# Kernel tuning notes

Measured on AMD Instinct MI355X. Metric: run time of the kernel, lower is better.

## Reference

```python
import jax, jax.numpy as jnp
import numpy as np

B, D, H, O = 8192, 1024, 2048, 1024   # batch, input_dim, hidden_dim, output_dim
T, NOPS = 4, 3                        # num_tempers, operators per bank (fixed at init)


def setup_inputs() -> dict:
    key = jax.random.key(0)
    ks = jax.random.split(key, 6)
    sc = 0.02
    return {
        "x": jax.random.normal(ks[0], (B, D), jnp.float32),
        # per-temper input_proj: Linear(D -> H)
        "Wp": jax.random.normal(ks[1], (T, H, D), jnp.float32) * sc,
        "bp": jnp.zeros((T, H), jnp.float32),
        "Wop": jax.random.normal(ks[2], (T, NOPS, H, H), jnp.float32) * sc,
        "bop": jnp.zeros((T, NOPS, H), jnp.float32),
        # routing_logits ~ randn per Temper.__init__
        "logits": jax.random.normal(ks[3], (T, NOPS), jnp.float32),
        # readout: Linear(T*H -> O)
        "Wr": jax.random.normal(ks[4], (O, T * H), jnp.float32) * sc,
        "br": jnp.zeros((O,), jnp.float32),
    }


def reference(x, Wp, bp, Wop, bop, logits, Wr, br):
    def temper(Wp_i, bp_i, Wop_i, bop_i, lg):
        # input projection: [B, H]
        xp = x @ Wp_i.T + bp_i
        # top-2 routing over operator bank (output is unweighted dispatch)
        w = jax.nn.softmax(lg)
        _, idx = jax.lax.top_k(w, 2)
        Wa, ba = Wop_i[idx[0]], bop_i[idx[0]]
        Wb, bb = Wop_i[idx[1]], bop_i[idx[1]]
        # each operator = Sequential(ReLU, Linear, ReLU)
        h = jax.nn.relu(jax.nn.relu(xp) @ Wa.T + ba)
        return jax.nn.relu(jax.nn.relu(h) @ Wb.T + bb)

    outs = jax.vmap(temper)(Wp, bp, Wop, bop, logits)          # [T, B, H]
    cat = jnp.transpose(outs, (1, 0, 2)).reshape(x.shape[0], -1)  # [B, T*H]
    return cat @ Wr.T + br                                      # [B, O]
```

## Files before the change

kernel.cpp:

```cpp
#include <hip/hip_runtime.h>

static constexpr int Bn = 8192;
static constexpr int Dd = 1024;
static constexpr int Hh = 2048;
static constexpr int Oo = 1024;
static constexpr int Tt = 4;
static constexpr int NO = 3;
#define TB 256

typedef __attribute__((ext_vector_type(8))) short bf16x8;
typedef __attribute__((ext_vector_type(4))) float f32x4;

__device__ __forceinline__ ushort f2bf(float f) {
  union { float f; unsigned u; } v; v.f = f;
  return (ushort)((v.u + 0x7FFFu + ((v.u >> 16) & 1u)) >> 16);
}

__global__ void top2_kernel(const float* __restrict__ logits, int* __restrict__ idx) {
  if (threadIdx.x == 0 && blockIdx.x == 0) {
    for (int t = 0; t < Tt; ++t) {
      const float* lg = logits + t * NO;
      int i0 = 0;
      for (int k = 1; k < NO; ++k) if (lg[k] > lg[i0]) i0 = k;
      int i1 = -1;
      for (int k = 0; k < NO; ++k) {
        if (k == i0) continue;
        if (i1 < 0 || lg[k] > lg[i1]) i1 = k;
      }
      idx[2 * t] = i0;
      idx[2 * t + 1] = i1;
    }
  }
}

__global__ void cvt_bf16(const float* __restrict__ src, ushort* __restrict__ dst, int n4) {
  int i = blockIdx.x * blockDim.x + threadIdx.x;
  if (i >= n4) return;
  float4 v = ((const float4*)src)[i];
  ((ushort4*)dst)[i] = make_ushort4(f2bf(v.x), f2bf(v.y), f2bf(v.z), f2bf(v.w));
}

__global__ void cvt_sel(const float* __restrict__ WopT, const int* __restrict__ idx2,
                        ushort* __restrict__ Wa, ushort* __restrict__ Wb, int n4) {
  int i = blockIdx.x * blockDim.x + threadIdx.x;
  if (i >= n4) return;
  size_t n = (size_t)n4 * 4;
  float4 va = ((const float4*)(WopT + (size_t)idx2[0] * n))[i];
  float4 vb = ((const float4*)(WopT + (size_t)idx2[1] * n))[i];
  ((ushort4*)Wa)[i] = make_ushort4(f2bf(va.x), f2bf(va.y), f2bf(va.z), f2bf(va.w));
  ((ushort4*)Wb)[i] = make_ushort4(f2bf(vb.x), f2bf(vb.y), f2bf(vb.z), f2bf(vb.w));
}

#define ISSUE_TILE(kk, p)                                                                   \
  do {                                                                                      \
    __builtin_amdgcn_global_load_lds(                                                       \
        (const __attribute__((address_space(1))) void*)(a0 + (kk)),                         \
        (__attribute__((address_space(3))) void*)(&As[p][w * 512]), 16, 0, 0);              \
    __builtin_amdgcn_global_load_lds(                                                       \
        (const __attribute__((address_space(1))) void*)(a1 + (kk)),                         \
        (__attribute__((address_space(3))) void*)(&As[p][2048 + w * 512]), 16, 0, 0);       \
    __builtin_amdgcn_global_load_lds(                                                       \
        (const __attribute__((address_space(1))) void*)(b0 + (kk)),                         \
        (__attribute__((address_space(3))) void*)(&Bs[p][w * 512]), 16, 0, 0);              \
    __builtin_amdgcn_global_load_lds(                                                       \
        (const __attribute__((address_space(1))) void*)(b1 + (kk)),                         \
        (__attribute__((address_space(3))) void*)(&Bs[p][2048 + w * 512]), 16, 0, 0);       \
  } while (0)

template <int EP>
__global__ __launch_bounds__(TB) void gemm_bt(
    const ushort* __restrict__ A, int lda,
    const ushort* __restrict__ B, int ldb,
    const float* __restrict__ bias, const int* __restrict__ idxp, int sel, int bstride,
    void* __restrict__ Cv, int ldc, int K) {
  __shared__ __align__(16) ushort As[2][128 * 32];
  __shared__ __align__(16) ushort Bs[2][128 * 32];
  const int tid = threadIdx.x;
  const int w = tid >> 6;
  const int lane = tid & 63;
  const int quad = lane >> 4;
  const int l16 = lane & 15;

  const int GX = gridDim.x, GY = gridDim.y;
  const int f = blockIdx.y * GX + blockIdx.x;
  const int xcd = f & 7;
  const int s = f >> 3;
  const int pxc = (GX >= 16) ? 2 : 1;
  const int pw = GX / pxc;
  const int ph = (GY * pxc) >> 3;
  const int bx = (xcd % pxc) * pw + (s % pw);
  const int by = (xcd / pxc) * ph + (s / pw);
  const int m0 = by * 128;
  const int n0 = bx * 128;
  const int wm = (w >> 1) * 64;
  const int wn = (w & 1) * 64;

  f32x4 acc[4][4];
#pragma unroll
  for (int i = 0; i < 4; ++i)
#pragma unroll
    for (int j = 0; j < 4; ++j)
#pragma unroll
      for (int r = 0; r < 4; ++r) acc[i][j][r] = 0.f;

  const int srow = tid >> 2;
  const int skc = ((tid & 3) ^ ((tid >> 3) & 3)) * 8;
  const ushort* a0 = A + (size_t)(m0 + srow) * lda + skc;
  const ushort* a1 = A + (size_t)(m0 + 64 + srow) * lda + skc;
  const ushort* b0 = B + (size_t)(n0 + srow) * ldb + skc;
  const ushort* b1 = B + (size_t)(n0 + 64 + srow) * ldb + skc;

  const int fq = (quad ^ ((l16 >> 1) & 3)) * 8;

  const int niter = K >> 5;
  ISSUE_TILE(0, 0);
  for (int it = 0; it < niter; ++it) {
    const int p = it & 1;
    __syncthreads();
    if (it + 1 < niter) ISSUE_TILE((it + 1) << 5, p ^ 1);

    bf16x8 af[4], bfr[4];
#pragma unroll
    for (int i = 0; i < 4; ++i)
      af[i] = *(const bf16x8*)&As[p][((wm >> 4) + i) * 512 + l16 * 32 + fq];
#pragma unroll
    for (int j = 0; j < 4; ++j)
      bfr[j] = *(const bf16x8*)&Bs[p][((wn >> 4) + j) * 512 + l16 * 32 + fq];
#pragma unroll
    for (int i = 0; i < 4; ++i)
#pragma unroll
      for (int j = 0; j < 4; ++j)
        acc[i][j] = __builtin_amdgcn_mfma_f32_16x16x32_bf16(af[i], bfr[j], acc[i][j], 0, 0, 0);
  }

  const float* bb = bias;
  if (EP == 0 && idxp) bb += (size_t)idxp[sel] * bstride;

#pragma unroll
  for (int i = 0; i < 4; ++i) {
#pragma unroll
    for (int j = 0; j < 4; ++j) {
      const int col = n0 + wn + j * 16 + l16;
      const float bv = (EP == 2) ? 0.f : bb[col];
#pragma unroll
      for (int r = 0; r < 4; ++r) {
        const int row = m0 + wm + i * 16 + quad * 4 + r;
        float v = acc[i][j][r] + bv;
        if (EP == 0) {
          v = v > 0.f ? v : 0.f;
          ((ushort*)Cv)[(size_t)row * ldc + col] = f2bf(v);
        } else if (EP == 1) {
          ((float*)Cv)[(size_t)row * ldc + col] = v;
        } else {
          ((float*)Cv)[(size_t)row * ldc + col] += v;
        }
      }
    }
  }
}

extern "C" void kernel_launch(void* const* d_in, const int* in_sizes, int n_in,
                              void* d_out, int out_size, void* d_ws, size_t ws_size,
                              hipStream_t stream) {
  const float* x      = (const float*)d_in[0];
  const float* Wp     = (const float*)d_in[1];
  const float* bp     = (const float*)d_in[2];
  const float* Wop    = (const float*)d_in[3];
  const float* bop    = (const float*)d_in[4];
  const float* logits = (const float*)d_in[5];
  const float* Wr     = (const float*)d_in[6];
  const float* br     = (const float*)d_in[7];
  float* out = (float*)d_out;

  char* ws = (char*)d_ws;
  size_t off = 0;
  int* idx = (int*)ws;                          off += 256;
  ushort* xb   = (ushort*)(ws + off);           off += (size_t)Bn * Dd * 2;
  ushort* WpB  = (ushort*)(ws + off);           off += (size_t)Tt * Hh * Dd * 2;
  ushort* WrB  = (ushort*)(ws + off);           off += (size_t)Oo * Tt * Hh * 2;
  ushort* WaB  = (ushort*)(ws + off);           off += (size_t)Hh * Hh * 2;
  ushort* WbB  = (ushort*)(ws + off);           off += (size_t)Hh * Hh * 2;
  ushort* bufA = (ushort*)(ws + off);           off += (size_t)Bn * Hh * 2;
  ushort* bufB = (ushort*)(ws + off);           off += (size_t)Bn * Hh * 2;

  top2_kernel<<<1, 64, 0, stream>>>(logits, idx);
  {
    int n4 = Bn * Dd / 4;
    cvt_bf16<<<(n4 + TB - 1) / TB, TB, 0, stream>>>(x, xb, n4);
  }
  {
    int n4 = Tt * Hh * Dd / 4;
    cvt_bf16<<<(n4 + TB - 1) / TB, TB, 0, stream>>>(Wp, WpB, n4);
  }
  {
    int n4 = Oo * Tt * Hh / 4;
    cvt_bf16<<<(n4 + TB - 1) / TB, TB, 0, stream>>>(Wr, WrB, n4);
  }

  dim3 gHB(Hh / 128, Bn / 128);
  dim3 gOB(Oo / 128, Bn / 128);

  for (int t = 0; t < Tt; ++t) {
    int n4 = Hh * Hh / 4;
    cvt_sel<<<(n4 + TB - 1) / TB, TB, 0, stream>>>(Wop + (size_t)t * NO * Hh * Hh, idx + 2 * t,
                                                   WaB, WbB, n4);
    gemm_bt<0><<<gHB, TB, 0, stream>>>(xb, Dd, WpB + (size_t)t * Hh * Dd, Dd,
                                       bp + (size_t)t * Hh, nullptr, 0, 0, bufA, Hh, Dd);
    gemm_bt<0><<<gHB, TB, 0, stream>>>(bufA, Hh, WaB, Hh,
                                       bop + (size_t)t * NO * Hh, idx + 2 * t, 0, Hh,
                                       bufB, Hh, Hh);
    gemm_bt<0><<<gHB, TB, 0, stream>>>(bufB, Hh, WbB, Hh,
                                       bop + (size_t)t * NO * Hh, idx + 2 * t, 1, Hh,
                                       bufA, Hh, Hh);
    if (t == 0)
      gemm_bt<1><<<gOB, TB, 0, stream>>>(bufA, Hh, WrB + (size_t)t * Hh, Tt * Hh,
                                         br, nullptr, 0, 0, out, Oo, Hh);
    else
      gemm_bt<2><<<gOB, TB, 0, stream>>>(bufA, Hh, WrB + (size_t)t * Hh, Tt * Hh,
                                         nullptr, nullptr, 0, 0, out, Oo, Hh);
  }
}
```

Baseline: 1.464 ms.

## Add 256x256 8-wave GEMM with ping-pong staged pipeline for hidden layers

Adds a new GEMM kernel using 256x256 output tiles with 512 threads, K-step 64, XOR-swizzled LDS and a hand-scheduled interleave of direct global-to-LDS loads, LDS reads and MFMA quadrants separated by barriers and priority hints. It replaces the 128x128 kernel for the three hidden-size GEMMs per temper to raise arithmetic intensity and overlap memory with compute. The larger tiles give only 256 workgroups per GEMM, which may underfill the GPU, and the heavy register and LDS use (64KB per block) limits occupancy.

```diff
diff --git a/kernel.cpp b/kernel.cpp
--- a/kernel.cpp
+++ b/kernel.cpp
@@ -159,6 +159,184 @@
   }
 }
 
+#define BAR() __builtin_amdgcn_s_barrier()
+#define SCHEDB() __builtin_amdgcn_sched_barrier(0)
+#define WAITLGKM() asm volatile("s_waitcnt lgkmcnt(0)" ::: "memory")
+#define WAITVM(N) asm volatile("s_waitcnt vmcnt(" #N ")" ::: "memory")
+
+#define STG(BASE, LD, ARR, P, H, KT)                                                        \
+  do {                                                                                      \
+    const int kt_ = ((KT) < ntile) ? (KT) : (ntile - 1);                                    \
+    const ushort* g_ = (BASE) + (size_t)(H) * 128 * (LD) + (size_t)kt_ * 64;                \
+    __builtin_amdgcn_global_load_lds(                                                       \
+        (const __attribute__((address_space(1))) void*)g_,                                  \
+        (__attribute__((address_space(3))) void*)&ARR[(P) * 16384 + (H) * 8192 + w * 512],  \
+        16, 0, 0);                                                                          \
+    __builtin_amdgcn_global_load_lds(                                                       \
+        (const __attribute__((address_space(1))) void*)(g_ + (size_t)64 * (LD)),            \
+        (__attribute__((address_space(3))) void*)&ARR[(P) * 16384 + (H) * 8192 + 4096 +     \
+                                                      w * 512],                             \
+        16, 0, 0);                                                                          \
+  } while (0)
+
+#define RD_A(P, MH)                                                                         \
+  do {                                                                                      \
+    _Pragma("unroll") for (int mf = 0; mf < 4; ++mf)                                        \
+    _Pragma("unroll") for (int kk = 0; kk < 2; ++kk)                                        \
+        af[mf][kk] = *(const bf16x8*)&As[(P) * 16384 + ak[kk] + ((MH) * 4 + mf) * 1024];    \
+  } while (0)
+
+#define RD_B(P, NH)                                                                         \
+  do {                                                                                      \
+    _Pragma("unroll") for (int nf = 0; nf < 2; ++nf)                                        \
+    _Pragma("unroll") for (int kk = 0; kk < 2; ++kk)                                        \
+        bfr[(NH) * 2 + nf][kk] =                                                            \
+            *(const bf16x8*)&Bs[(P) * 16384 + bk[kk] + ((NH) * 2 + nf) * 1024];             \
+  } while (0)
+
+#define MFMA_Q(MH, NH)                                                                      \
+  do {                                                                                      \
+    __builtin_amdgcn_s_setprio(1);                                                          \
+    _Pragma("unroll") for (int mf = 0; mf < 4; ++mf)                                        \
+    _Pragma("unroll") for (int nf = 0; nf < 2; ++nf)                                        \
+    _Pragma("unroll") for (int kk = 0; kk < 2; ++kk)                                        \
+        acc[(MH) * 4 + mf][(NH) * 2 + nf] = __builtin_amdgcn_mfma_f32_16x16x32_bf16(        \
+            af[mf][kk], bfr[(NH) * 2 + nf][kk], acc[(MH) * 4 + mf][(NH) * 2 + nf], 0, 0, 0);\
+    __builtin_amdgcn_s_setprio(0);                                                          \
+  } while (0)
+
+template <int EP>
+__global__ __launch_bounds__(512, 2) void gemm256(
+    const ushort* __restrict__ A, int lda,
+    const ushort* __restrict__ B, int ldb,
+    const float* __restrict__ bias, const int* __restrict__ idxp, int sel, int bstride,
+    void* __restrict__ Cv, int ldc, int K) {
+  __shared__ __align__(16) ushort As[32768];
+  __shared__ __align__(16) ushort Bs[32768];
+  const int tid = threadIdx.x;
+  const int w = tid >> 6;
+  const int lane = tid & 63;
+  const int quad = lane >> 4;
+  const int l16 = lane & 15;
+  const int wr = w >> 2;
+  const int wc = w & 3;
+
+  const int GX = gridDim.x;
+  const int nwg = GX * gridDim.y;
+  const int fid = blockIdx.y * GX + blockIdx.x;
+  const int q8 = nwg >> 3, r8 = nwg & 7, xcd = fid & 7, ser = fid >> 3;
+  const int wg = (xcd < r8 ? xcd * (q8 + 1) : r8 * (q8 + 1) + (xcd - r8) * q8) + ser;
+  const int m0 = (wg / GX) * 256;
+  const int n0 = (wg % GX) * 256;
+
+  f32x4 acc[8][4];
+#pragma unroll
+  for (int i = 0; i < 8; ++i)
+#pragma unroll
+    for (int j = 0; j < 4; ++j)
+#pragma unroll
+      for (int r = 0; r < 4; ++r) acc[i][j][r] = 0.f;
+
+  const int srow = tid >> 3;
+  const int scol = (tid & 7) ^ (srow & 7);
+  const ushort* Abase = A + (size_t)(m0 + srow) * lda + scol * 8;
+  const ushort* Bbase = B + (size_t)(n0 + srow) * ldb + scol * 8;
+  const int ntile = K >> 6;
+  const int ni = ntile >> 1;
+
+  int ak[2], bk[2];
+#pragma unroll
+  for (int kk = 0; kk < 2; ++kk) {
+    const int ch = ((kk * 4 + quad) ^ (l16 & 7)) * 8;
+    ak[kk] = wr * 8192 + l16 * 64 + ch;
+    bk[kk] = (wc >> 1) * 8192 + ((wc & 1) * 64 + l16) * 64 + ch;
+  }
+
+  STG(Abase, lda, As, 0, 0, 0);
+  STG(Abase, lda, As, 0, 1, 0);
+  STG(Bbase, ldb, Bs, 0, 0, 0);
+  STG(Bbase, ldb, Bs, 0, 1, 0);
+  STG(Bbase, ldb, Bs, 1, 0, 1);
+  STG(Bbase, ldb, Bs, 1, 1, 1);
+  WAITVM(4);
+  BAR();
+  SCHEDB();
+
+  bf16x8 af[4][2], bfr[4][2];
+  for (int i = 0; i < ni; ++i) {
+    const int t = 2 * i;
+    RD_A(0, 0); RD_B(0, 0);
+    STG(Abase, lda, As, 1, 0, t + 1);
+    BAR(); WAITLGKM();
+    MFMA_Q(0, 0);
+    BAR();
+    RD_B(0, 1);
+    STG(Abase, lda, As, 1, 1, t + 1);
+    BAR(); WAITLGKM();
+    MFMA_Q(0, 1);
+    BAR();
+    RD_A(0, 1);
+    STG(Bbase, ldb, Bs, 0, 0, t + 2);
+    BAR(); WAITLGKM();
+    MFMA_Q(1, 0);
+    BAR();
+    STG(Bbase, ldb, Bs, 0, 1, t + 2);
+    WAITVM(4);
+    BAR();
+    SCHEDB();
+    MFMA_Q(1, 1);
+    BAR();
+    RD_A(1, 0); RD_B(1, 0);
+    STG(Abase, lda, As, 0, 0, t + 2);
+    BAR(); WAITLGKM();
+    MFMA_Q(0, 0);
+    BAR();
+    RD_B(1, 1);
+    STG(Abase, lda, As, 0, 1, t + 2);
+    BAR(); WAITLGKM();
+    MFMA_Q(0, 1);
+    BAR();
+    RD_A(1, 1);
+    STG(Bbase, ldb, Bs, 1, 0, t + 3);
+    BAR(); WAITLGKM();
+    MFMA_Q(1, 0);
+    BAR();
+    STG(Bbase, ldb, Bs, 1, 1, t + 3);
+    WAITVM(4);
+    BAR();
+    SCHEDB();
+    MFMA_Q(1, 1);
+    BAR();
+  }
+  WAITVM(0);
+  BAR();
+
+  const float* bb = bias;
+  if (EP == 0 && idxp) bb += (size_t)idxp[sel] * bstride;
+
+#pragma unroll
+  for (int mf = 0; mf < 8; ++mf) {
+#pragma unroll
+    for (int nf = 0; nf < 4; ++nf) {
+      const int col = n0 + wc * 64 + nf * 16 + l16;
+      const float bv = (EP == 2) ? 0.f : bb[col];
+#pragma unroll
+      for (int r = 0; r < 4; ++r) {
+        const int row = m0 + wr * 128 + mf * 16 + quad * 4 + r;
+        float v = acc[mf][nf][r] + bv;
+        if (EP == 0) {
+          v = v > 0.f ? v : 0.f;
+          ((ushort*)Cv)[(size_t)row * ldc + col] = f2bf(v);
+        } else if (EP == 1) {
+          ((float*)Cv)[(size_t)row * ldc + col] = v;
+        } else {
+          ((float*)Cv)[(size_t)row * ldc + col] += v;
+        }
+      }
+    }
+  }
+}
+
 extern "C" void kernel_launch(void* const* d_in, const int* in_sizes, int n_in,
                               void* d_out, int out_size, void* d_ws, size_t ws_size,
                               hipStream_t stream) {
@@ -197,21 +375,21 @@
     cvt_bf16<<<(n4 + TB - 1) / TB, TB, 0, stream>>>(Wr, WrB, n4);
   }
 
-  dim3 gHB(Hh / 128, Bn / 128);
+  dim3 g256(Hh / 256, Bn / 256);
   dim3 gOB(Oo / 128, Bn / 128);
 
   for (int t = 0; t < Tt; ++t) {
     int n4 = Hh * Hh / 4;
     cvt_sel<<<(n4 + TB - 1) / TB, TB, 0, stream>>>(Wop + (size_t)t * NO * Hh * Hh, idx + 2 * t,
                                                    WaB, WbB, n4);
-    gemm_bt<0><<<gHB, TB, 0, stream>>>(xb, Dd, WpB + (size_t)t * Hh * Dd, Dd,
-                                       bp + (size_t)t * Hh, nullptr, 0, 0, bufA, Hh, Dd);
-    gemm_bt<0><<<gHB, TB, 0, stream>>>(bufA, Hh, WaB, Hh,
-                                       bop + (size_t)t * NO * Hh, idx + 2 * t, 0, Hh,
-                                       bufB, Hh, Hh);
-    gemm_bt<0><<<gHB, TB, 0, stream>>>(bufB, Hh, WbB, Hh,
-                                       bop + (size_t)t * NO * Hh, idx + 2 * t, 1, Hh,
-                                       bufA, Hh, Hh);
+    gemm256<0><<<g256, 512, 0, stream>>>(xb, Dd, WpB + (size_t)t * Hh * Dd, Dd,
+                                         bp + (size_t)t * Hh, nullptr, 0, 0, bufA, Hh, Dd);
+    gemm256<0><<<g256, 512, 0, stream>>>(bufA, Hh, WaB, Hh,
+                                         bop + (size_t)t * NO * Hh, idx + 2 * t, 0, Hh,
+                                         bufB, Hh, Hh);
+    gemm256<0><<<g256, 512, 0, stream>>>(bufB, Hh, WbB, Hh,
+                                         bop + (size_t)t * NO * Hh, idx + 2 * t, 1, Hh,
+                                         bufA, Hh, Hh);
     if (t == 0)
       gemm_bt<1><<<gOB, TB, 0, stream>>>(bufA, Hh, WrB + (size_t)t * Hh, Tt * Hh,
                                          br, nullptr, 0, 0, out, Oo, Hh);
```

Result: faster. 1.216 ms (-16.9%).
